# Kernel tuning notes

Measured on AMD Instinct MI355X. Metric: run time of the kernel, lower is better.

## Reference

```python
import jax, jax.numpy as jnp
import numpy as np

V, E, H, L = 512, 128, 256, 4
B, T = 128, 1024


def setup_inputs() -> dict:
    key = jax.random.key(0)
    ks = jax.random.split(key, 16)
    s = 0.05
    inp = {
        "x": jax.random.randint(ks[0], (B, T), 0, V),
        "tags": jax.random.randint(ks[1], (B, T), 0, L),
        "mask": jnp.ones((B, T), dtype=bool),
        "emb": jax.random.normal(ks[2], (V, E), jnp.float32) * s,
        "w_ih_f": jax.random.normal(ks[3], (3 * H, E), jnp.float32) * s,
        "w_hh_f": jax.random.normal(ks[4], (3 * H, H), jnp.float32) * s,
        "b_ih_f": jax.random.normal(ks[5], (3 * H,), jnp.float32) * s,
        "b_hh_f": jax.random.normal(ks[6], (3 * H,), jnp.float32) * s,
        "w_ih_b": jax.random.normal(ks[7], (3 * H, E), jnp.float32) * s,
        "w_hh_b": jax.random.normal(ks[8], (3 * H, H), jnp.float32) * s,
        "b_ih_b": jax.random.normal(ks[9], (3 * H,), jnp.float32) * s,
        "b_hh_b": jax.random.normal(ks[10], (3 * H,), jnp.float32) * s,
        "fc_w": jax.random.normal(ks[11], (L, 2 * H), jnp.float32) * s,
        "fc_b": jax.random.normal(ks[12], (L,), jnp.float32) * s,
        "start_trans": jax.random.normal(ks[13], (L,), jnp.float32) * 0.1,
        "end_trans": jax.random.normal(ks[14], (L,), jnp.float32) * 0.1,
        "trans": jax.random.normal(ks[15], (L, L), jnp.float32) * 0.1,
    }
    return inp


def _gru_scan(xe, w_ih, w_hh, b_ih, b_hh):
    # xe: [B,T,E] -> out [B,T,H]; PyTorch GRU gate order: r, z, n
    gi = jnp.einsum("bte,ge->btg", xe, w_ih) + b_ih  # [B,T,3H]
    gi = jnp.swapaxes(gi, 0, 1)  # [T,B,3H]
    h0 = jnp.zeros((xe.shape[0], H), xe.dtype)

    def step(h, gi_t):
        gh = h @ w_hh.T + b_hh
        i_r, i_z, i_n = jnp.split(gi_t, 3, axis=-1)
        h_r, h_z, h_n = jnp.split(gh, 3, axis=-1)
        r = jax.nn.sigmoid(i_r + h_r)
        z = jax.nn.sigmoid(i_z + h_z)
        n = jnp.tanh(i_n + r * h_n)
        h_new = (1.0 - z) * n + z * h
        return h_new, h_new

    _, out = jax.lax.scan(step, h0, gi)
    return jnp.swapaxes(out, 0, 1)  # [B,T,H]


def _crf_neg_llh(emissions, tags, mask, start_trans, end_trans, trans):
    # emissions [B,T,L], tags [B,T] int, mask [B,T] bool
    maskf = mask.astype(emissions.dtype)
    # ----- numerator: score of gold path -----
    em_sel = jnp.take_along_axis(emissions, tags[..., None], axis=2)[..., 0]  # [B,T]
    trans_sel = trans[tags[:, :-1], tags[:, 1:]]  # [B,T-1]
    score = start_trans[tags[:, 0]] + em_sel[:, 0]
    score = score + jnp.sum((trans_sel + em_sel[:, 1:]) * maskf[:, 1:], axis=1)
    seq_ends = jnp.sum(mask.astype(jnp.int32), axis=1) - 1  # [B]
    last_tags = jnp.take_along_axis(tags, seq_ends[:, None], axis=1)[:, 0]
    score = score + end_trans[last_tags]
    # ----- denominator: forward algorithm (logsumexp scan) -----
    alpha0 = start_trans[None, :] + emissions[:, 0]  # [B,L]
    em_rest = jnp.swapaxes(emissions[:, 1:], 0, 1)  # [T-1,B,L]
    m_rest = jnp.swapaxes(mask[:, 1:], 0, 1)  # [T-1,B]

    def step(alpha, inputs):
        emit_t, m_t = inputs
        nxt = jax.nn.logsumexp(alpha[:, :, None] + trans[None] + emit_t[:, None, :], axis=1)
        alpha = jnp.where(m_t[:, None], nxt, alpha)
        return alpha, None

    alpha, _ = jax.lax.scan(step, alpha0, (em_rest, m_rest))
    logZ = jax.nn.logsumexp(alpha + end_trans[None, :], axis=1)  # [B]
    llh = score - logZ
    return -jnp.mean(llh)  # reduction='mean', negated in Segmenter.forward


def reference(x, tags, mask, emb, w_ih_f, w_hh_f, b_ih_f, b_hh_f,
              w_ih_b, w_hh_b, b_ih_b, b_hh_b, fc_w, fc_b,
              start_trans, end_trans, trans):
    xe = emb[x]  # [B,T,E]
    out_f = _gru_scan(xe, w_ih_f, w_hh_f, b_ih_f, b_hh_f)
    out_b = _gru_scan(xe[:, ::-1], w_ih_b, w_hh_b, b_ih_b, b_hh_b)[:, ::-1]
    gru_out = jnp.concatenate([out_f, out_b], axis=-1)  # [B,T,2H]
    emissions = jnp.einsum("bth,lh->btl", gru_out, fc_w) + fc_b  # [B,T,L]
    return _crf_neg_llh(emissions, tags, mask, start_trans, end_trans, trans)
```

## Files before the change

### kernel.cpp

```cpp
#include <hip/hip_runtime.h>
#include <hip/hip_fp16.h>

#define Tn 1024
#define NB 128

typedef _Float16 h2_t __attribute__((ext_vector_type(2)));

__device__ __forceinline__ float dot2f(h2_t a, h2_t b, float c) {
#if __has_builtin(__builtin_amdgcn_fdot2)
  return __builtin_amdgcn_fdot2(a, b, c, false);
#else
  return c + (float)a[0] * (float)b[0] + (float)a[1] * (float)b[1];
#endif
}

__device__ __forceinline__ h2_t u2h(unsigned u) {
  union { unsigned u; h2_t h; } c; c.u = u; return c.h;
}

__device__ __forceinline__ float dpp_xor1(float v) {
  int i = __builtin_bit_cast(int, v);
  return __builtin_bit_cast(float, __builtin_amdgcn_update_dpp(i, i, 0xB1, 0xF, 0xF, true));
}
__device__ __forceinline__ float dpp_xor2(float v) {
  int i = __builtin_bit_cast(int, v);
  return __builtin_bit_cast(float, __builtin_amdgcn_update_dpp(i, i, 0x4E, 0xF, 0xF, true));
}

__global__ __launch_bounds__(768)
void gv_build(const float* __restrict__ emb,
              const float* __restrict__ wihf, const float* __restrict__ bihf,
              const float* __restrict__ wihb, const float* __restrict__ bihb,
              float* __restrict__ gv)
{
  const int d  = blockIdx.x >> 7;
  const int v4 = (blockIdx.x & 127) * 4;
  const float* wih = d ? wihb : wihf;
  const float* bih = d ? bihb : bihf;
  __shared__ float se[4][128];
  const int tid = threadIdx.x;
  if (tid < 512) se[tid >> 7][tid & 127] = emb[(v4 + (tid >> 7)) * 128 + (tid & 127)];
  __syncthreads();
  const int row = tid;
  const float b0 = bih[row];
  float a0 = b0, a1 = b0, a2 = b0, a3 = b0;
  #pragma unroll
  for (int e = 0; e < 128; e += 4) {
    const float4 w = *reinterpret_cast<const float4*>(&wih[row * 128 + e]);
    a0 = fmaf(w.x, se[0][e], a0); a0 = fmaf(w.y, se[0][e+1], a0);
    a0 = fmaf(w.z, se[0][e+2], a0); a0 = fmaf(w.w, se[0][e+3], a0);
    a1 = fmaf(w.x, se[1][e], a1); a1 = fmaf(w.y, se[1][e+1], a1);
    a1 = fmaf(w.z, se[1][e+2], a1); a1 = fmaf(w.w, se[1][e+3], a1);
    a2 = fmaf(w.x, se[2][e], a2); a2 = fmaf(w.y, se[2][e+1], a2);
    a2 = fmaf(w.z, se[2][e+2], a2); a2 = fmaf(w.w, se[2][e+3], a2);
    a3 = fmaf(w.x, se[3][e], a3); a3 = fmaf(w.y, se[3][e+1], a3);
    a3 = fmaf(w.z, se[3][e+2], a3); a3 = fmaf(w.w, se[3][e+3], a3);
  }
  float* out = gv + (size_t)(d * 512 + v4) * 768 + row;
  out[0] = a0; out[768] = a1; out[1536] = a2; out[2304] = a3;
}

__global__ __launch_bounds__(768, 3)
void gru_scan(const int* __restrict__ x,
              const float* __restrict__ gv,
              const float* __restrict__ whhf,
              const float* __restrict__ whhb,
              const float* __restrict__ bhhf,
              const float* __restrict__ bhhb,
              const float* __restrict__ fcw,
              float* __restrict__ em)
{
  const int tid = threadIdx.x;
  const int rid = tid >> 2;
  const int q   = tid & 3;
  const int dir = blockIdx.x & 1;
  const int b   = blockIdx.x >> 1;

  const float* whh = dir ? whhb : whhf;
  const float* bhh = dir ? bhhb : bhhf;

  __shared__ __align__(16) char hls[2][576];
  __shared__ float dls[768];
  __shared__ __align__(8) _Float16 fcs[4][256];

  h2_t w[128];
  #pragma unroll
  for (int i = 0; i < 4; ++i) {
    const float* wrow = whh + (size_t)(4 * rid + i) * 256 + q * 64;
    #pragma unroll
    for (int c = 0; c < 16; ++c) {
      const float4 f = reinterpret_cast<const float4*>(wrow)[c];
      h2_t a; a[0] = (_Float16)f.x; a[1] = (_Float16)f.y;
      h2_t bb; bb[0] = (_Float16)f.z; bb[1] = (_Float16)f.w;
      w[i * 32 + 2 * c] = a;
      w[i * 32 + 2 * c + 1] = bb;
    }
  }
  float4 bias = make_float4(0.f, 0.f, 0.f, 0.f);
  if (q == 0) bias = *reinterpret_cast<const float4*>(bhh + 4 * rid);

  for (int i = tid; i < 1024; i += 768)
    fcs[i >> 8][i & 255] = (_Float16)fcw[(i >> 8) * 512 + dir * 256 + (i & 255)];
  if (tid < 144) reinterpret_cast<uint2*>(hls)[tid] = make_uint2(0, 0);
  __syncthreads();

  const float* gvd = gv + (size_t)dir * (512 * 768);
  const int*   xb  = x + b * Tn;
  float*       emo = em + (size_t)(dir * NB + b) * (Tn * 4);

  const bool updt = tid < 256;
  float ho = 0.f;
  int tok = updt ? xb[dir ? (Tn - 1) : 0] : 0;

  for (int t = 0; t < Tn; ++t) {
    const int cur = t & 1;

    float gir = 0.f, giz = 0.f, gin = 0.f;
    int ntok = 0;
    if (updt) {
      const float* g = gvd + (size_t)tok * 768 + tid;
      gir = g[0]; giz = g[256]; gin = g[512];
      ntok = xb[(t + 1 < Tn) ? (dir ? (Tn - 2 - t) : (t + 1)) : 0];
    }

    const char* hbase = hls[cur] + q * 144;
    float a0 = bias.x, a1 = bias.y, a2 = bias.z, a3 = bias.w;
    #pragma unroll
    for (int c = 0; c < 8; ++c) {
      const uint4 hq = *reinterpret_cast<const uint4*>(hbase + c * 16);
      const h2_t h0 = u2h(hq.x), h1 = u2h(hq.y), h2v = u2h(hq.z), h3 = u2h(hq.w);
      a0 = dot2f(w[     4*c+0], h0, a0); a0 = dot2f(w[     4*c+1], h1, a0);
      a0 = dot2f(w[     4*c+2], h2v, a0); a0 = dot2f(w[     4*c+3], h3, a0);
      a1 = dot2f(w[32 + 4*c+0], h0, a1); a1 = dot2f(w[32 + 4*c+1], h1, a1);
      a1 = dot2f(w[32 + 4*c+2], h2v, a1); a1 = dot2f(w[32 + 4*c+3], h3, a1);
      a2 = dot2f(w[64 + 4*c+0], h0, a2); a2 = dot2f(w[64 + 4*c+1], h1, a2);
      a2 = dot2f(w[64 + 4*c+2], h2v, a2); a2 = dot2f(w[64 + 4*c+3], h3, a2);
      a3 = dot2f(w[96 + 4*c+0], h0, a3); a3 = dot2f(w[96 + 4*c+1], h1, a3);
      a3 = dot2f(w[96 + 4*c+2], h2v, a3); a3 = dot2f(w[96 + 4*c+3], h3, a3);
    }
    a0 += dpp_xor1(a0); a0 += dpp_xor2(a0);
    a1 += dpp_xor1(a1); a1 += dpp_xor2(a1);
    a2 += dpp_xor1(a2); a2 += dpp_xor2(a2);
    a3 += dpp_xor1(a3); a3 += dpp_xor2(a3);
    const float v01 = (q & 1) ? a1 : a0;
    const float v23 = (q & 1) ? a3 : a2;
    dls[tid] = (q & 2) ? v23 : v01;
    __syncthreads();

    if (updt) {
      const float dr = dls[tid], dz = dls[tid + 256], dn = dls[tid + 512];
      const float r    = 1.f / (1.f + __expf(-(gir + dr)));
      const float z    = 1.f / (1.f + __expf(-(giz + dz)));
      const float npre = gin + r * dn;
      const float e2   = __expf(-2.f * npre);
      const float n    = (1.f - e2) / (1.f + e2);
      const float hnew = (1.f - z) * n + z * ho;
      ho = hnew;
      tok = ntok;
      *reinterpret_cast<_Float16*>(hls[cur ^ 1] + (tid >> 6) * 144 + (tid & 63) * 2) =
          (_Float16)hnew;
    } else if (tid < 512 && t > 0) {
      const int e = tid - 256, l = e >> 6, p = e & 63;
      const uint2 hq = *reinterpret_cast<const uint2*>(hls[cur] + (p >> 4) * 144 + (p & 15) * 8);
      const h2_t* fr = reinterpret_cast<const h2_t*>(&fcs[l][0]);
      float a = dot2f(fr[2 * p], u2h(hq.x), 0.f);
      a = dot2f(fr[2 * p + 1], u2h(hq.y), a);
      a += __shfl_xor(a, 1);  a += __shfl_xor(a, 2);  a += __shfl_xor(a, 4);
      a += __shfl_xor(a, 8);  a += __shfl_xor(a, 16); a += __shfl_xor(a, 32);
      if (p == 0) {
        const int ptt = dir ? (Tn - t) : (t - 1);
        emo[ptt * 4 + l] = a;
      }
    }
    __syncthreads();
  }

  if (tid >= 256 && tid < 512) {
    const int e = tid - 256, l = e >> 6, p = e & 63;
    const uint2 hq = *reinterpret_cast<const uint2*>(hls[Tn & 1] + (p >> 4) * 144 + (p & 15) * 8);
    const h2_t* fr = reinterpret_cast<const h2_t*>(&fcs[l][0]);
    float a = dot2f(fr[2 * p], u2h(hq.x), 0.f);
    a = dot2f(fr[2 * p + 1], u2h(hq.y), a);
    a += __shfl_xor(a, 1);  a += __shfl_xor(a, 2);  a += __shfl_xor(a, 4);
    a += __shfl_xor(a, 8);  a += __shfl_xor(a, 16); a += __shfl_xor(a, 32);
    if (p == 0) {
      const int ptt = dir ? 0 : (Tn - 1);
      emo[ptt * 4 + l] = a;
    }
  }
}

__global__ __launch_bounds__(64)
void crf_nllh(const int* __restrict__ tags,
              const float* __restrict__ em,
              const float* __restrict__ fc_b,
              const float* __restrict__ st,
              const float* __restrict__ et,
              const float* __restrict__ tr,
              float* __restrict__ llh)
{
  const int lane = threadIdx.x;
  const int l = lane & 3;
  const int q = lane >> 2;
  const int b = blockIdx.x * 16 + q;
  const float* ef = em + (size_t)b * Tn * 4;
  const float* eb = em + ((size_t)NB + b) * Tn * 4;
  const int* tg = tags + b * Tn;
  const float fcb = fc_b[l];
  const float tc0 = tr[l * 4 + l];
  const float tc1 = tr[(l ^ 1) * 4 + l];
  const float tc2 = tr[(l ^ 2) * 4 + l];
  const float tc3 = tr[(l ^ 3) * 4 + l];

  const float e0 = ef[l] + eb[l] + fcb;
  float alpha = st[l] + e0;
  int tprev = tg[0];
  float score = (tprev == l) ? (st[l] + e0) : 0.f;

  #pragma unroll 8
  for (int t = 1; t < Tn; ++t) {
    const float e = ef[t * 4 + l] + eb[t * 4 + l] + fcb;
    const int tc = tg[t];
    if (tc == l) {
      const int s2 = tprev ^ l;
      const float tsel = (s2 & 1) ? ((s2 & 2) ? tc3 : tc1)
                                  : ((s2 & 2) ? tc2 : tc0);
      score += e + tsel;
    }
    tprev = tc;
    const float a1 = __shfl_xor(alpha, 1);
    const float a2 = __shfl_xor(alpha, 2);
    const float a3 = __shfl_xor(alpha, 3);
    const float v0 = alpha + tc0;
    const float v1 = a1 + tc1;
    const float v2 = a2 + tc2;
    const float v3 = a3 + tc3;
    const float mx = fmaxf(fmaxf(v0, v1), fmaxf(v2, v3));
    const float s = __expf(v0 - mx) + __expf(v1 - mx) + __expf(v2 - mx) + __expf(v3 - mx);
    alpha = mx + __logf(s) + e;
  }

  score += (tprev == l) ? et[l] : 0.f;
  float ae = alpha + et[l];
  float m1 = fmaxf(ae, __shfl_xor(ae, 1));
  m1 = fmaxf(m1, __shfl_xor(m1, 2));
  float se = __expf(ae - m1);
  se += __shfl_xor(se, 1);
  se += __shfl_xor(se, 2);
  const float logZ = m1 + __logf(se);
  float sc = score + __shfl_xor(score, 1);
  sc += __shfl_xor(sc, 2);
  if (l == 0) llh[b] = sc - logZ;
}

__global__ __launch_bounds__(128)
void reduce_mean(const float* __restrict__ llh, float* __restrict__ out)
{
  const int t = threadIdx.x;
  float v = llh[t];
  #pragma unroll
  for (int m = 32; m >= 1; m >>= 1) v += __shfl_xor(v, m);
  __shared__ float s2[2];
  if ((t & 63) == 0) s2[t >> 6] = v;
  __syncthreads();
  if (t == 0) out[0] = -(s2[0] + s2[1]) * (1.f / 128.f);
}

extern "C" void kernel_launch(void* const* d_in, const int* in_sizes, int n_in,
                              void* d_out, int out_size, void* d_ws, size_t ws_size,
                              hipStream_t stream) {
  const int*   x    = (const int*)d_in[0];
  const int*   tags = (const int*)d_in[1];
  const float* emb  = (const float*)d_in[3];
  const float* wihf = (const float*)d_in[4];
  const float* whhf = (const float*)d_in[5];
  const float* bihf = (const float*)d_in[6];
  const float* bhhf = (const float*)d_in[7];
  const float* wihb = (const float*)d_in[8];
  const float* whhb = (const float*)d_in[9];
  const float* bihb = (const float*)d_in[10];
  const float* bhhb = (const float*)d_in[11];
  const float* fcw  = (const float*)d_in[12];
  const float* fcb  = (const float*)d_in[13];
  const float* st   = (const float*)d_in[14];
  const float* et   = (const float*)d_in[15];
  const float* tr   = (const float*)d_in[16];

  char* ws = (char*)d_ws;
  float* gv  = (float*)ws;
  float* em  = (float*)(ws + 3145728);
  float* llh = (float*)(ws + 3145728 + 4194304);

  gv_build<<<dim3(256), dim3(768), 0, stream>>>(emb, wihf, bihf, wihb, bihb, gv);
  gru_scan<<<dim3(256), dim3(768), 0, stream>>>(x, gv, whhf, whhb, bhhf, bhhb, fcw, em);
  crf_nllh<<<dim3(8), dim3(64), 0, stream>>>(tags, em, fcb, st, et, tr, llh);
  reduce_mean<<<dim3(1), dim3(128), 0, stream>>>(llh, (float*)d_out);
}
```

Before: 1.655 ms.

## Restructure GRU scan: 2 threads per hidden unit, one barrier per step

Reorganises the recurrent kernel so each hidden unit is handled by two threads, each holding half of the r/z/n weight rows in fp16 registers. Gate preactivations are reduced with one shuffle rather than written to shared memory, which removes the second __syncthreads per timestep. The exp2 scaling constants and the r/z hidden biases are folded into the precomputed input-gate table and the weights, so the gates can use native exp2 and rcp. The emission projection is now written one step late through a small double buffer. The cost is high register pressure from 384 fp16 weights per thread, the block size drops to 512, and the approximate math functions may lose some accuracy.

Result: slower. 1.829 ms (+10.5%).

```diff
diff --git a/kernel.cpp b/kernel.cpp
--- a/kernel.cpp
+++ b/kernel.cpp
@@ -4,7 +4,11 @@
 #define Tn 1024
 #define NB 128
 
-typedef _Float16 h2_t __attribute__((ext_vector_type(2)));
+#define S_RZ (-1.4426950408889634f)
+#define S_N  (-2.8853900817779268f)
+
+typedef _Float16 h2_t  __attribute__((ext_vector_type(2)));
+typedef _Float16 f16x8 __attribute__((ext_vector_type(8)));
 
 __device__ __forceinline__ float dot2f(h2_t a, h2_t b, float c) {
 #if __has_builtin(__builtin_amdgcn_fdot2)
@@ -18,25 +22,17 @@
   union { unsigned u; h2_t h; } c; c.u = u; return c.h;
 }
 
-__device__ __forceinline__ float dpp_xor1(float v) {
-  int i = __builtin_bit_cast(int, v);
-  return __builtin_bit_cast(float, __builtin_amdgcn_update_dpp(i, i, 0xB1, 0xF, 0xF, true));
-}
-__device__ __forceinline__ float dpp_xor2(float v) {
-  int i = __builtin_bit_cast(int, v);
-  return __builtin_bit_cast(float, __builtin_amdgcn_update_dpp(i, i, 0x4E, 0xF, 0xF, true));
-}
-
 __global__ __launch_bounds__(768)
 void gv_build(const float* __restrict__ emb,
-              const float* __restrict__ wihf, const float* __restrict__ bihf,
-              const float* __restrict__ wihb, const float* __restrict__ bihb,
+              const float* __restrict__ wihf, const float* __restrict__ bihf, const float* __restrict__ bhhf,
+              const float* __restrict__ wihb, const float* __restrict__ bihb, const float* __restrict__ bhhb,
               float* __restrict__ gv)
 {
   const int d  = blockIdx.x >> 7;
   const int v4 = (blockIdx.x & 127) * 4;
   const float* wih = d ? wihb : wihf;
   const float* bih = d ? bihb : bihf;
+  const float* bhh = d ? bhhb : bhhf;
   __shared__ float se[4][128];
   const int tid = threadIdx.x;
   if (tid < 512) se[tid >> 7][tid & 127] = emb[(v4 + (tid >> 7)) * 128 + (tid & 127)];
@@ -56,11 +52,34 @@
     a3 = fmaf(w.x, se[3][e], a3); a3 = fmaf(w.y, se[3][e+1], a3);
     a3 = fmaf(w.z, se[3][e+2], a3); a3 = fmaf(w.w, se[3][e+3], a3);
   }
+  const float sc  = (row < 512) ? S_RZ : S_N;
+  const float add = (row < 512) ? bhh[row] : 0.f;
   float* out = gv + (size_t)(d * 512 + v4) * 768 + row;
-  out[0] = a0; out[768] = a1; out[1536] = a2; out[2304] = a3;
-}
-
-__global__ __launch_bounds__(768, 3)
+  out[0]    = sc * (a0 + add);
+  out[768]  = sc * (a1 + add);
+  out[1536] = sc * (a2 + add);
+  out[2304] = sc * (a3 + add);
+}
+
+#define DW(i) f16x8 WR##i, WZ##i, WN##i;
+#define PKG(G, SC, i) { \
+  const float4 _a = *reinterpret_cast<const float4*>(row##G + 8 * i); \
+  const float4 _c = *reinterpret_cast<const float4*>(row##G + 8 * i + 4); \
+  W##G##i[0] = (_Float16)(_a.x * (SC)); W##G##i[1] = (_Float16)(_a.y * (SC)); \
+  W##G##i[2] = (_Float16)(_a.z * (SC)); W##G##i[3] = (_Float16)(_a.w * (SC)); \
+  W##G##i[4] = (_Float16)(_c.x * (SC)); W##G##i[5] = (_Float16)(_c.y * (SC)); \
+  W##G##i[6] = (_Float16)(_c.z * (SC)); W##G##i[7] = (_Float16)(_c.w * (SC)); }
+#define PK3(i) PKG(R, S_RZ, i) PKG(Z, S_RZ, i) PKG(N, S_N, i)
+#define SL(v, a, b) (__builtin_shufflevector(v, v, a, b))
+#define DOT(i) { \
+  const uint4 _hq = *reinterpret_cast<const uint4*>(hrow + 16 * i); \
+  const h2_t _h0 = u2h(_hq.x), _h1 = u2h(_hq.y), _h2 = u2h(_hq.z), _h3 = u2h(_hq.w); \
+  ar = dot2f(SL(WR##i,0,1), _h0, ar); az = dot2f(SL(WZ##i,0,1), _h0, az); an = dot2f(SL(WN##i,0,1), _h0, an); \
+  ar = dot2f(SL(WR##i,2,3), _h1, ar); az = dot2f(SL(WZ##i,2,3), _h1, az); an = dot2f(SL(WN##i,2,3), _h1, an); \
+  ar = dot2f(SL(WR##i,4,5), _h2, ar); az = dot2f(SL(WZ##i,4,5), _h2, az); an = dot2f(SL(WN##i,4,5), _h2, an); \
+  ar = dot2f(SL(WR##i,6,7), _h3, ar); az = dot2f(SL(WZ##i,6,7), _h3, az); an = dot2f(SL(WN##i,6,7), _h3, an); }
+
+__global__ __launch_bounds__(512, 2)
 void gru_scan(const int* __restrict__ x,
               const float* __restrict__ gv,
               const float* __restrict__ whhf,
@@ -70,123 +89,131 @@
               const float* __restrict__ fcw,
               float* __restrict__ em)
 {
-  const int tid = threadIdx.x;
-  const int rid = tid >> 2;
-  const int q   = tid & 3;
-  const int dir = blockIdx.x & 1;
-  const int b   = blockIdx.x >> 1;
+  const int tid  = threadIdx.x;
+  const int j    = tid >> 1;
+  const int half = tid & 1;
+  const int dir  = blockIdx.x & 1;
+  const int b    = blockIdx.x >> 1;
 
   const float* whh = dir ? whhb : whhf;
   const float* bhh = dir ? bhhb : bhhf;
 
-  __shared__ __align__(16) char hls[2][576];
-  __shared__ float dls[768];
-  __shared__ __align__(8) _Float16 fcs[4][256];
-
-  h2_t w[128];
-  #pragma unroll
-  for (int i = 0; i < 4; ++i) {
-    const float* wrow = whh + (size_t)(4 * rid + i) * 256 + q * 64;
-    #pragma unroll
-    for (int c = 0; c < 16; ++c) {
-      const float4 f = reinterpret_cast<const float4*>(wrow)[c];
-      h2_t a; a[0] = (_Float16)f.x; a[1] = (_Float16)f.y;
-      h2_t bb; bb[0] = (_Float16)f.z; bb[1] = (_Float16)f.w;
-      w[i * 32 + 2 * c] = a;
-      w[i * 32 + 2 * c + 1] = bb;
-    }
-  }
-  float4 bias = make_float4(0.f, 0.f, 0.f, 0.f);
-  if (q == 0) bias = *reinterpret_cast<const float4*>(bhh + 4 * rid);
-
-  for (int i = tid; i < 1024; i += 768)
-    fcs[i >> 8][i & 255] = (_Float16)fcw[(i >> 8) * 512 + dir * 256 + (i & 255)];
-  if (tid < 144) reinterpret_cast<uint2*>(hls)[tid] = make_uint2(0, 0);
-  __syncthreads();
+  __shared__ __align__(16) char hls[2 * 544];
+  __shared__ float els[2][8];
+
+  if (tid < 68) reinterpret_cast<uint4*>(hls)[tid] = make_uint4(0, 0, 0, 0);
+
+  DW(0) DW(1) DW(2) DW(3) DW(4) DW(5) DW(6) DW(7)
+  DW(8) DW(9) DW(10) DW(11) DW(12) DW(13) DW(14) DW(15)
+  {
+    const float* rowR = whh + (size_t)j * 256 + half * 128;
+    const float* rowZ = rowR + 256 * 256;
+    const float* rowN = rowZ + 256 * 256;
+    PK3(0) PK3(1) PK3(2) PK3(3)
+    __builtin_amdgcn_sched_barrier(0);
+    PK3(4) PK3(5) PK3(6) PK3(7)
+    __builtin_amdgcn_sched_barrier(0);
+    PK3(8) PK3(9) PK3(10) PK3(11)
+    __builtin_amdgcn_sched_barrier(0);
+    PK3(12) PK3(13) PK3(14) PK3(15)
+    __builtin_amdgcn_sched_barrier(0);
+  }
+
+  const float bn2 = 0.5f * S_N * bhh[512 + j];
+
+  const int w8 = tid >> 6;
+  const int kh = w8 >> 2;
+  const int p  = (tid & 63) >> 1;
+  h2_t fe0, fe1;
+  {
+    const float4 f = *reinterpret_cast<const float4*>(
+        fcw + (w8 & 3) * 512 + dir * 256 + kh * 128 + 4 * p);
+    fe0[0] = (_Float16)f.x; fe0[1] = (_Float16)f.y;
+    fe1[0] = (_Float16)f.z; fe1[1] = (_Float16)f.w;
+  }
+  const int kh_off = kh * 272 + 8 * p;
+  const int hr_off = half * 272;
+  const int hw_off = (j >> 7) * 272 + (j & 127) * 2;
 
   const float* gvd = gv + (size_t)dir * (512 * 768);
   const int*   xb  = x + b * Tn;
   float*       emo = em + (size_t)(dir * NB + b) * (Tn * 4);
 
-  const bool updt = tid < 256;
   float ho = 0.f;
-  int tok = updt ? xb[dir ? (Tn - 1) : 0] : 0;
+  int tok = xb[dir ? (Tn - 1) : 0];
+  __syncthreads();
 
   for (int t = 0; t < Tn; ++t) {
     const int cur = t & 1;
 
     float gir = 0.f, giz = 0.f, gin = 0.f;
-    int ntok = 0;
-    if (updt) {
-      const float* g = gvd + (size_t)tok * 768 + tid;
+    if (!half) {
+      const float* g = gvd + (size_t)tok * 768 + j;
       gir = g[0]; giz = g[256]; gin = g[512];
-      ntok = xb[(t + 1 < Tn) ? (dir ? (Tn - 2 - t) : (t + 1)) : 0];
     }
-
-    const char* hbase = hls[cur] + q * 144;
-    float a0 = bias.x, a1 = bias.y, a2 = bias.z, a3 = bias.w;
-    #pragma unroll
-    for (int c = 0; c < 8; ++c) {
-      const uint4 hq = *reinterpret_cast<const uint4*>(hbase + c * 16);
-      const h2_t h0 = u2h(hq.x), h1 = u2h(hq.y), h2v = u2h(hq.z), h3 = u2h(hq.w);
-      a0 = dot2f(w[     4*c+0], h0, a0); a0 = dot2f(w[     4*c+1], h1, a0);
-      a0 = dot2f(w[     4*c+2], h2v, a0); a0 = dot2f(w[     4*c+3], h3, a0);
-      a1 = dot2f(w[32 + 4*c+0], h0, a1); a1 = dot2f(w[32 + 4*c+1], h1, a1);
-      a1 = dot2f(w[32 + 4*c+2], h2v, a1); a1 = dot2f(w[32 + 4*c+3], h3, a1);
-      a2 = dot2f(w[64 + 4*c+0], h0, a2); a2 = dot2f(w[64 + 4*c+1], h1, a2);
-      a2 = dot2f(w[64 + 4*c+2], h2v, a2); a2 = dot2f(w[64 + 4*c+3], h3, a2);
-      a3 = dot2f(w[96 + 4*c+0], h0, a3); a3 = dot2f(w[96 + 4*c+1], h1, a3);
-      a3 = dot2f(w[96 + 4*c+2], h2v, a3); a3 = dot2f(w[96 + 4*c+3], h3, a3);
+    const int ntok = xb[dir ? (t + 2 <= Tn ? Tn - 2 - t : 0)
+                           : (t + 1 < Tn ? t + 1 : 0)];
+
+    if (t >= 2 && tid < 4) {
+      const float v = els[cur ^ 1][tid] + els[cur ^ 1][tid + 4];
+      const int ptt = dir ? (Tn - (t - 1)) : (t - 2);
+      emo[ptt * 4 + tid] = v;
     }
-    a0 += dpp_xor1(a0); a0 += dpp_xor2(a0);
-    a1 += dpp_xor1(a1); a1 += dpp_xor2(a1);
-    a2 += dpp_xor1(a2); a2 += dpp_xor2(a2);
-    a3 += dpp_xor1(a3); a3 += dpp_xor2(a3);
-    const float v01 = (q & 1) ? a1 : a0;
-    const float v23 = (q & 1) ? a3 : a2;
-    dls[tid] = (q & 2) ? v23 : v01;
+
+    const char* hrow = hls + cur * 544 + hr_off;
+    float ar = 0.f, az = 0.f, an = bn2;
+    DOT(0) DOT(1) DOT(2) DOT(3)
+    __builtin_amdgcn_sched_barrier(0);
+    DOT(4) DOT(5) DOT(6) DOT(7)
+    __builtin_amdgcn_sched_barrier(0);
+    DOT(8) DOT(9) DOT(10) DOT(11)
+    __builtin_amdgcn_sched_barrier(0);
+    DOT(12) DOT(13) DOT(14) DOT(15)
+
+    ar += __shfl_xor(ar, 1);
+    az += __shfl_xor(az, 1);
+    an += __shfl_xor(an, 1);
+
+    if (!half) {
+      const float er = __builtin_amdgcn_exp2f(gir + ar);
+      const float r  = __builtin_amdgcn_rcpf(1.f + er);
+      const float ez = __builtin_amdgcn_exp2f(giz + az);
+      const float z  = __builtin_amdgcn_rcpf(1.f + ez);
+      float y = fmaf(r, an, gin);
+      y = fminf(y, 126.f);
+      const float en = __builtin_amdgcn_exp2f(y);
+      const float n  = (1.f - en) * __builtin_amdgcn_rcpf(1.f + en);
+      const float hnew = fmaf(z, ho - n, n);
+      ho = hnew;
+      *reinterpret_cast<_Float16*>(hls + (cur ^ 1) * 544 + hw_off) = (_Float16)hnew;
+    } else if (t > 0) {
+      const uint2 hq = *reinterpret_cast<const uint2*>(hls + cur * 544 + kh_off);
+      float pa = dot2f(fe0, u2h(hq.x), 0.f);
+      pa = dot2f(fe1, u2h(hq.y), pa);
+      pa += __shfl_xor(pa, 2);  pa += __shfl_xor(pa, 4);  pa += __shfl_xor(pa, 8);
+      pa += __shfl_xor(pa, 16); pa += __shfl_xor(pa, 32);
+      if ((tid & 63) == 1) els[t & 1][w8] = pa;
+    }
+    tok = ntok;
     __syncthreads();
-
-    if (updt) {
-      const float dr = dls[tid], dz = dls[tid + 256], dn = dls[tid + 512];
-      const float r    = 1.f / (1.f + __expf(-(gir + dr)));
-      const float z    = 1.f / (1.f + __expf(-(giz + dz)));
-      const float npre = gin + r * dn;
-      const float e2   = __expf(-2.f * npre);
-      const float n    = (1.f - e2) / (1.f + e2);
-      const float hnew = (1.f - z) * n + z * ho;
-      ho = hnew;
-      tok = ntok;
-      *reinterpret_cast<_Float16*>(hls[cur ^ 1] + (tid >> 6) * 144 + (tid & 63) * 2) =
-          (_Float16)hnew;
-    } else if (tid < 512 && t > 0) {
-      const int e = tid - 256, l = e >> 6, p = e & 63;
-      const uint2 hq = *reinterpret_cast<const uint2*>(hls[cur] + (p >> 4) * 144 + (p & 15) * 8);
-      const h2_t* fr = reinterpret_cast<const h2_t*>(&fcs[l][0]);
-      float a = dot2f(fr[2 * p], u2h(hq.x), 0.f);
-      a = dot2f(fr[2 * p + 1], u2h(hq.y), a);
-      a += __shfl_xor(a, 1);  a += __shfl_xor(a, 2);  a += __shfl_xor(a, 4);
-      a += __shfl_xor(a, 8);  a += __shfl_xor(a, 16); a += __shfl_xor(a, 32);
-      if (p == 0) {
-        const int ptt = dir ? (Tn - t) : (t - 1);
-        emo[ptt * 4 + l] = a;
-      }
-    }
-    __syncthreads();
-  }
-
-  if (tid >= 256 && tid < 512) {
-    const int e = tid - 256, l = e >> 6, p = e & 63;
-    const uint2 hq = *reinterpret_cast<const uint2*>(hls[Tn & 1] + (p >> 4) * 144 + (p & 15) * 8);
-    const h2_t* fr = reinterpret_cast<const h2_t*>(&fcs[l][0]);
-    float a = dot2f(fr[2 * p], u2h(hq.x), 0.f);
-    a = dot2f(fr[2 * p + 1], u2h(hq.y), a);
-    a += __shfl_xor(a, 1);  a += __shfl_xor(a, 2);  a += __shfl_xor(a, 4);
-    a += __shfl_xor(a, 8);  a += __shfl_xor(a, 16); a += __shfl_xor(a, 32);
-    if (p == 0) {
-      const int ptt = dir ? 0 : (Tn - 1);
-      emo[ptt * 4 + l] = a;
-    }
+  }
+
+  if (tid < 4) {
+    const float v = els[1][tid] + els[1][tid + 4];
+    emo[(dir ? 1 : (Tn - 2)) * 4 + tid] = v;
+  }
+  if (half) {
+    const uint2 hq = *reinterpret_cast<const uint2*>(hls + kh_off);
+    float pa = dot2f(fe0, u2h(hq.x), 0.f);
+    pa = dot2f(fe1, u2h(hq.y), pa);
+    pa += __shfl_xor(pa, 2);  pa += __shfl_xor(pa, 4);  pa += __shfl_xor(pa, 8);
+    pa += __shfl_xor(pa, 16); pa += __shfl_xor(pa, 32);
+    if ((tid & 63) == 1) els[0][w8] = pa;
+  }
+  __syncthreads();
+  if (tid < 4) {
+    const float v = els[0][tid] + els[0][tid + 4];
+    emo[(dir ? 0 : (Tn - 1)) * 4 + tid] = v;
   }
 }
 
@@ -291,8 +318,8 @@
   float* em  = (float*)(ws + 3145728);
   float* llh = (float*)(ws + 3145728 + 4194304);
 
-  gv_build<<<dim3(256), dim3(768), 0, stream>>>(emb, wihf, bihf, wihb, bihb, gv);
-  gru_scan<<<dim3(256), dim3(768), 0, stream>>>(x, gv, whhf, whhb, bhhf, bhhb, fcw, em);
+  gv_build<<<dim3(256), dim3(768), 0, stream>>>(emb, wihf, bihf, bhhf, wihb, bihb, bhhb, gv);
+  gru_scan<<<dim3(256), dim3(512), 0, stream>>>(x, gv, whhf, whhb, bhhf, bhhb, fcw, em);
   crf_nllh<<<dim3(8), dim3(64), 0, stream>>>(tags, em, fcb, st, et, tr, llh);
   reduce_mean<<<dim3(1), dim3(128), 0, stream>>>(llh, (float*)d_out);
 }
```
